# Kernel tuning notes

Measured on AMD Instinct MI355X. Metric: run time of the kernel, lower is better.

Reference implementation:

```python
import jax, jax.numpy as jnp
import numpy as np

B, N, D = 4, 2048, 1024
H = 16
HD = D // H


def setup_inputs() -> dict:
    key = jax.random.key(0)
    ks = jax.random.split(key, 7)
    bound_w = 1.0 / np.sqrt(D)  # kaiming_uniform(a=sqrt(5)) on (D, D) -> U(-1/sqrt(fan_in), 1/sqrt(fan_in))
    x = jax.random.normal(ks[0], (B, N, D), dtype=jnp.float32)
    Wq = jax.random.uniform(ks[1], (D, D), jnp.float32, -bound_w, bound_w)
    Wk = jax.random.uniform(ks[2], (D, D), jnp.float32, -bound_w, bound_w)
    Wv = jax.random.uniform(ks[3], (D, D), jnp.float32, -bound_w, bound_w)
    Wo = jax.random.uniform(ks[4], (D, D), jnp.float32, -bound_w, bound_w)
    bo = jax.random.uniform(ks[5], (D,), jnp.float32, -bound_w, bound_w)
    return {"x": x, "Wq": Wq, "Wk": Wk, "Wv": Wv, "Wo": Wo, "bo": bo}


def reference(x, Wq, Wk, Wv, Wo, bo):
    b, n, _ = x.shape
    # QKV projections: contraction over W's FIRST axis, matching torch einsum 'bnd,di->bni'
    Q = jnp.einsum('bnd,di->bni', x, Wq)
    K = jnp.einsum('bnd,di->bni', x, Wk)
    V = jnp.einsum('bnd,di->bni', x, Wv)
    # split heads: [b, h, n, hd]
    Q = Q.reshape(b, n, H, HD).transpose(0, 2, 1, 3)
    K = K.reshape(b, n, H, HD).transpose(0, 2, 1, 3)
    V = V.reshape(b, n, H, HD).transpose(0, 2, 1, 3)
    scores = jnp.einsum('bhnd,bhmd->bhnm', Q, K) / np.sqrt(HD).astype(np.float32)
    causal = jnp.triu(jnp.ones((n, n), dtype=bool), k=1)  # True above diagonal -> masked
    scores = jnp.where(causal[None, None, :, :], -jnp.inf, scores)
    attn = jax.nn.softmax(scores, axis=-1)
    # dropout rate is 0.0 -> identity
    ctx = jnp.einsum('bhnm,bhmd->bhnd', attn, V)
    ctx = ctx.transpose(0, 2, 1, 3).reshape(b, n, D)
    return ctx @ Wo.T + bo
```

## Files before the change

### kernel.cpp

```cpp
#include <hip/hip_runtime.h>
#include <hip/hip_bf16.h>

typedef __bf16 bf16;
typedef __bf16 bf16x4 __attribute__((ext_vector_type(4)));
typedef __bf16 bf16x8 __attribute__((ext_vector_type(8)));
typedef float  f32x4  __attribute__((ext_vector_type(4)));

#define B_  4
#define N_  2048
#define D_  1024
#define H_  16
#define HD_ 64

#define QSCALE 0.1803368801111204f

__device__ __forceinline__ bf16x8 ld8(const bf16* p) {
  return *reinterpret_cast<const bf16x8*>(p);
}

__device__ __forceinline__ void gload16(const bf16* g, bf16* l) {
  __builtin_amdgcn_global_load_lds(
      (const __attribute__((address_space(1))) void*)g,
      (__attribute__((address_space(3))) void*)l, 16, 0, 0);
}

__global__ __launch_bounds__(256) void cast_k(const float* __restrict__ in,
                                              bf16* __restrict__ out, int n) {
  int i = (blockIdx.x * 256 + threadIdx.x) * 8;
  if (i >= n) return;
  float4 a = *reinterpret_cast<const float4*>(in + i);
  float4 b = *reinterpret_cast<const float4*>(in + i + 4);
  bf16x8 o;
  o[0] = (bf16)a.x; o[1] = (bf16)a.y; o[2] = (bf16)a.z; o[3] = (bf16)a.w;
  o[4] = (bf16)b.x; o[5] = (bf16)b.y; o[6] = (bf16)b.z; o[7] = (bf16)b.w;
  *reinterpret_cast<bf16x8*>(out + i) = o;
}

__global__ __launch_bounds__(1024)
void transpose3_k(const float* __restrict__ w0, const float* __restrict__ w1,
                  const float* __restrict__ w2, bf16* __restrict__ out) {
  __shared__ float t[32][33];
  const int z = blockIdx.z;
  const float* in = (z == 0) ? w0 : (z == 1) ? w1 : w2;
  const float scale = (z == 0) ? QSCALE : 1.0f;
  bf16* o = out + (size_t)z * D_ * D_;
  int c = blockIdx.x * 32 + threadIdx.x;
  int r = blockIdx.y * 32 + threadIdx.y;
  t[threadIdx.y][threadIdx.x] = in[r * D_ + c];
  __syncthreads();
  int oc = blockIdx.y * 32 + threadIdx.x;
  int orr = blockIdx.x * 32 + threadIdx.y;
  o[orr * D_ + oc] = (bf16)(scale * t[threadIdx.x][threadIdx.y]);
}

#define GEMM_CORE(A_, Bt_, K_)                                                    \
  f32x4 acc[4][4] = {};                                                           \
  const int srow = wid * 16 + (lane >> 2);                \
  const int schk = ((lane & 3) ^ ((lane >> 4) & 3)) * 8;         \
  const int q8   = ((lane >> 4) ^ (l15 >> 2)) * 8;              \
  _Pragma("unroll")                                                               \
  for (int j = 0; j < 2; ++j) {                                                   \
    gload16(&(A_)[(size_t)(brow + j * 64 + srow) * (K_) + schk],                  \
            &As[(j * 64 + wid * 16) * 32]);                                       \
    gload16(&(Bt_)[(size_t)(bcol + j * 64 + srow) * (K_) + schk],                 \
            &Bs[(j * 64 + wid * 16) * 32]);                                       \
  }                                                                               \
  _Pragma("unroll")                                                               \
  for (int j = 0; j < 2; ++j) {                                                   \
    gload16(&(A_)[(size_t)(brow + j * 64 + srow) * (K_) + 32 + schk],             \
            &As[4096 + (j * 64 + wid * 16) * 32]);                                \
    gload16(&(Bt_)[(size_t)(bcol + j * 64 + srow) * (K_) + 32 + schk],            \
            &Bs[4096 + (j * 64 + wid * 16) * 32]);                                \
  }                                                                               \
  const int NIT = (K_) / 32;                                                      \
  int cur = 0, pre = 2;                                                           \
  for (int t = 0; t < NIT; ++t) {                                                 \
    asm volatile("s_barrier" ::: "memory");             \
    __builtin_amdgcn_sched_barrier(0);                                            \
    if (t + 2 < NIT) {                                                            \
      const int kk = (t + 2) * 32;                                                \
      _Pragma("unroll")                                                           \
      for (int j = 0; j < 2; ++j) {                                               \
        gload16(&(A_)[(size_t)(brow + j * 64 + srow) * (K_) + kk + schk],         \
                &As[pre * 4096 + (j * 64 + wid * 16) * 32]);                      \
        gload16(&(Bt_)[(size_t)(bcol + j * 64 + srow) * (K_) + kk + schk],        \
                &Bs[pre * 4096 + (j * 64 + wid * 16) * 32]);                      \
      }                                                                           \
      asm volatile("s_waitcnt vmcnt(8)" ::: "memory");                            \
    } else if (t + 1 < NIT) {                                                     \
      asm volatile("s_waitcnt vmcnt(4)" ::: "memory");                            \
    } else {                                                                      \
      asm volatile("s_waitcnt vmcnt(0)" ::: "memory");                            \
    }                                                                             \
    asm volatile("s_barrier" ::: "memory");             \
    __builtin_amdgcn_sched_barrier(0);                                            \
    const bf16* Ac = &As[cur * 4096];                                             \
    const bf16* Bc = &Bs[cur * 4096];                                             \
    bf16x8 af[4], bfr[4];                                                         \
    _Pragma("unroll")                                                             \
    for (int m = 0; m < 4; ++m)                                                   \
      af[m] = *reinterpret_cast<const bf16x8*>(&Ac[(wr + m * 16 + l15) * 32 + q8]); \
    _Pragma("unroll")                                                             \
    for (int n = 0; n < 4; ++n)                                                   \
      bfr[n] = *reinterpret_cast<const bf16x8*>(&Bc[(wc + n * 16 + l15) * 32 + q8]); \
    _Pragma("unroll")                                                             \
    for (int m = 0; m < 4; ++m)                                                   \
      _Pragma("unroll")                                                           \
      for (int n = 0; n < 4; ++n)                                                 \
        acc[m][n] = __builtin_amdgcn_mfma_f32_16x16x32_bf16(af[m], bfr[n],        \
                                                            acc[m][n], 0, 0, 0);  \
    cur = (cur == 2) ? 0 : cur + 1;                                               \
    pre = (pre == 2) ? 0 : pre + 1;                                               \
  }

__global__ __launch_bounds__(256, 3)
void gemm_qkv(const bf16* __restrict__ A, const bf16* __restrict__ Bt,
              bf16* __restrict__ qb, bf16* __restrict__ kb, bf16* __restrict__ vtb)
{
  __shared__ bf16 As[3 * 128 * 32];
  __shared__ bf16 Bs[3 * 128 * 32];
  const int tid  = threadIdx.x;
  const int lane = tid & 63;
  const int wid  = tid >> 6;
  const int wg   = blockIdx.x;
  const int xcd  = wg & 7;
  const int idx  = wg >> 3;
  const int brow = ((xcd << 3) + (idx & 7)) * 128;
  const int bcol = (idx >> 3) * 128;
  const int wr   = (wid >> 1) * 64;
  const int wc   = (wid & 1) * 64;
  const int l15  = lane & 15;
  const int g    = lane >> 4;

  GEMM_CORE(A, Bt, D_)

  const int which = bcol >> 10;
  const int r0 = g * 4;
  if (which == 2) {
#pragma unroll
    for (int m = 0; m < 4; ++m)
#pragma unroll
      for (int n = 0; n < 4; ++n) {
        int nn0  = brow + wr + m * 16 + r0;
        int gcol = (bcol & 1023) + wc + n * 16 + l15;
        int b = nn0 >> 11, nn = nn0 & (N_ - 1);
        int h = gcol >> 6, hd = gcol & 63;
        bf16x4 o;
#pragma unroll
        for (int r = 0; r < 4; ++r) o[r] = (bf16)acc[m][n][r];
        *reinterpret_cast<bf16x4*>(
            &vtb[((size_t)((b * H_ + h) * HD_ + hd)) * N_ + nn]) = o;
      }
  } else {
    bf16* outp = (which == 0) ? qb : kb;
#pragma unroll
    for (int m = 0; m < 4; ++m)
#pragma unroll
      for (int n = 0; n < 4; ++n)
#pragma unroll
        for (int r = 0; r < 4; ++r) {
          int grow = brow + wr + m * 16 + r0 + r;
          int gcol = (bcol & 1023) + wc + n * 16 + l15;
          int b = grow >> 11, nn = grow & (N_ - 1);
          int h = gcol >> 6, hd = gcol & 63;
          outp[((((size_t)(b * H_ + h)) * N_ + nn) << 6) + hd] = (bf16)acc[m][n][r];
        }
  }
}

__global__ __launch_bounds__(256, 3)
void gemm_out(const bf16* __restrict__ A, const bf16* __restrict__ Bt,
              float* __restrict__ C, const float* __restrict__ bias)
{
  __shared__ bf16 As[3 * 128 * 32];
  __shared__ bf16 Bs[3 * 128 * 32];
  const int tid  = threadIdx.x;
  const int lane = tid & 63;
  const int wid  = tid >> 6;
  const int wg   = blockIdx.x;
  const int xcd  = wg & 7;
  const int idx  = wg >> 3;
  const int brow = ((xcd << 3) + (idx & 7)) * 128;
  const int bcol = (idx >> 3) * 128;
  const int wr   = (wid >> 1) * 64;
  const int wc   = (wid & 1) * 64;
  const int l15  = lane & 15;
  const int g    = lane >> 4;

  GEMM_CORE(A, Bt, D_)

  const int r0 = g * 4;
#pragma unroll
  for (int m = 0; m < 4; ++m)
#pragma unroll
    for (int n = 0; n < 4; ++n)
#pragma unroll
      for (int r = 0; r < 4; ++r) {
        int grow = brow + wr + m * 16 + r0 + r;
        int gcol = bcol + wc + n * 16 + l15;
        C[(size_t)grow * D_ + gcol] = acc[m][n][r] + bias[gcol];
      }
}

__global__ __launch_bounds__(256, 3)
void attn_k(const bf16* __restrict__ q, const bf16* __restrict__ k,
            const bf16* __restrict__ vt, bf16* __restrict__ ctx)
{
  __shared__ bf16 Ks[2][64 * 64];
  __shared__ bf16 Vs[2][64 * 64];
  __shared__ bf16 Pl[4][2][16][72];
  const int tid  = threadIdx.x;
  const int lane = tid & 63;
  const int wid  = tid >> 6;
  const int bid  = blockIdx.x;
  const int bh   = bid & 63;
  const int c    = 15 - (bid >> 6);
  const int l15  = lane & 15;
  const int g    = lane >> 4;
  const int lk   = g * 8;
  const int swz  = (l15 & 7) << 4;

  const bf16* kp = k  + (size_t)bh * N_ * HD_;
  const bf16* vp = vt + (size_t)bh * HD_ * N_;
  const int b = bh >> 4, h = bh & 15;

  const int sr8   = lane >> 3;
  const int scoff = ((lane & 7) ^ sr8) * 8;

  bf16x8 ones8;
#pragma unroll
  for (int i = 0; i < 8; ++i) ones8[i] = (bf16)1.0f;

  const int qbase = c * 128 + wid * 32;
  const int nt    = 2 * c + 2;
  const int tm    = 2 * c + (wid >> 1);

  const bf16* qp = q + ((size_t)bh * N_ + qbase) * HD_;
  bf16x8 aq[2][2];
#pragma unroll
  for (int m = 0; m < 2; ++m)
#pragma unroll
    for (int c2 = 0; c2 < 2; ++c2)
      aq[m][c2] = ld8(qp + (size_t)(m * 16 + l15) * HD_ + c2 * 32 + lk);

  f32x4 oacc[2][5] = {};

#pragma unroll
  for (int j = 0; j < 2; ++j) {
    const int rr = j * 32 + wid * 8 + sr8;
    gload16(kp + (size_t)rr * HD_ + scoff, &Ks[0][(j * 32 + wid * 8) * 64]);
    gload16(vp + (size_t)rr * N_ + scoff, &Vs[0][(j * 32 + wid * 8) * 64]);
  }

  for (int t = 0; t < nt; ++t) {
    const int cur = t & 1;
    asm volatile("s_barrier" ::: "memory");
    __builtin_amdgcn_sched_barrier(0);
    if (t + 1 < nt) {
      const int kb = (t + 1) * 64;
#pragma unroll
      for (int j = 0; j < 2; ++j) {
        const int rr = j * 32 + wid * 8 + sr8;
        gload16(kp + (size_t)(kb + rr) * HD_ + scoff,
                &Ks[cur ^ 1][(j * 32 + wid * 8) * 64]);
        gload16(vp + (size_t)rr * N_ + kb + scoff,
                &Vs[cur ^ 1][(j * 32 + wid * 8) * 64]);
      }
      asm volatile("s_waitcnt vmcnt(4)" ::: "memory");
    } else {
      asm volatile("s_waitcnt vmcnt(0)" ::: "memory");
    }
    asm volatile("s_barrier" ::: "memory");
    __builtin_amdgcn_sched_barrier(0);

    if (t <= tm) {
      const char* kb_ = (const char*)&Ks[cur][0];
      const char* vb_ = (const char*)&Vs[cur][0];

      f32x4 s[2][4] = {};
#pragma unroll
      for (int tt = 0; tt < 4; ++tt) {
        bf16x8 bk0 = *reinterpret_cast<const bf16x8*>(
            kb_ + (tt * 16 + l15) * 128 + ((g * 16) ^ swz));
        bf16x8 bk1 = *reinterpret_cast<const bf16x8*>(
            kb_ + (tt * 16 + l15) * 128 + ((64 + g * 16) ^ swz));
#pragma unroll
        for (int m = 0; m < 2; ++m) {
          s[m][tt] = __builtin_amdgcn_mfma_f32_16x16x32_bf16(bk0, aq[m][0], s[m][tt], 0, 0, 0);
          s[m][tt] = __builtin_amdgcn_mfma_f32_16x16x32_bf16(bk1, aq[m][1], s[m][tt], 0, 0, 0);
        }
      }

      if (t == tm) {
#pragma unroll
        for (int m = 0; m < 2; ++m) {
          const int qr = qbase + m * 16 + l15;
#pragma unroll
          for (int tt = 0; tt < 4; ++tt)
#pragma unroll
            for (int r = 0; r < 4; ++r) {
              int kq = t * 64 + tt * 16 + g * 4 + r;
              if (kq > qr) s[m][tt][r] = -1e30f;
            }
        }
      }

#pragma unroll
      for (int m = 0; m < 2; ++m) {
#pragma unroll
        for (int tt = 0; tt < 4; ++tt)
#pragma unroll
          for (int r = 0; r < 4; ++r) s[m][tt][r] = exp2f(s[m][tt][r]);

#pragma unroll
        for (int tt = 0; tt < 4; ++tt) {
          bf16x4 pk;
#pragma unroll
          for (int r = 0; r < 4; ++r) pk[r] = (bf16)s[m][tt][r];
          *reinterpret_cast<bf16x4*>(&Pl[wid][m][l15][tt * 16 + g * 4]) = pk;
        }
      }

#pragma unroll
      for (int kc = 0; kc < 2; ++kc) {
        bf16x8 pb[2];
#pragma unroll
        for (int m = 0; m < 2; ++m)
          pb[m] = *reinterpret_cast<const bf16x8*>(&Pl[wid][m][l15][kc * 32 + lk]);
#pragma unroll
        for (int n = 0; n < 4; ++n) {
          bf16x8 vf = *reinterpret_cast<const bf16x8*>(
              vb_ + (n * 16 + l15) * 128 + ((kc * 64 + g * 16) ^ swz));
#pragma unroll
          for (int m = 0; m < 2; ++m)
            oacc[m][n] = __builtin_amdgcn_mfma_f32_16x16x32_bf16(vf, pb[m], oacc[m][n], 0, 0, 0);
        }
#pragma unroll
        for (int m = 0; m < 2; ++m)
          oacc[m][4] = __builtin_amdgcn_mfma_f32_16x16x32_bf16(ones8, pb[m], oacc[m][4], 0, 0, 0);
      }
    }
  }

#pragma unroll
  for (int m = 0; m < 2; ++m) {
    float inv = 1.f / oacc[m][4][0];
    bf16* cp = ctx + ((size_t)b * N_ + qbase + m * 16 + l15) * D_ + h * HD_;
#pragma unroll
    for (int n = 0; n < 4; ++n) {
      bf16x4 o;
#pragma unroll
      for (int r = 0; r < 4; ++r) o[r] = (bf16)(oacc[m][n][r] * inv);
      *reinterpret_cast<bf16x4*>(cp + n * 16 + g * 4) = o;
    }
  }
}

extern "C" void kernel_launch(void* const* d_in, const int* in_sizes, int n_in,
                              void* d_out, int out_size, void* d_ws, size_t ws_size,
                              hipStream_t stream)
{
  const float* x  = (const float*)d_in[0];
  const float* Wq = (const float*)d_in[1];
  const float* Wk = (const float*)d_in[2];
  const float* Wv = (const float*)d_in[3];
  const float* Wo = (const float*)d_in[4];
  const float* bo = (const float*)d_in[5];
  float* out = (float*)d_out;

  const size_t SZ_BHND = (size_t)B_ * H_ * N_ * HD_ * sizeof(bf16);
  const size_t SZ_W    = (size_t)D_ * D_ * sizeof(bf16);
  char* ws = (char*)d_ws;
  bf16* xbf  = (bf16*)(ws);
  bf16* ctx  = (bf16*)(ws);
  bf16* qb   = (bf16*)(ws + SZ_BHND);
  bf16* kbf  = (bf16*)(ws + 2 * SZ_BHND);
  bf16* vtb  = (bf16*)(ws + 3 * SZ_BHND);
  bf16* wqkv = (bf16*)(ws + 4 * SZ_BHND);
  bf16* wob  = (bf16*)(ws + 4 * SZ_BHND + 3 * SZ_W);
  if (ws_size < 4 * SZ_BHND + 4 * SZ_W) return;

  const int NX = B_ * N_ * D_;
  cast_k<<<NX / (256 * 8), 256, 0, stream>>>(x, xbf, NX);
  cast_k<<<(D_ * D_) / (256 * 8), 256, 0, stream>>>(Wo, wob, D_ * D_);

  transpose3_k<<<dim3(32, 32, 3), dim3(32, 32), 0, stream>>>(Wq, Wk, Wv, wqkv);

  gemm_qkv<<<1536, 256, 0, stream>>>(xbf, wqkv, qb, kbf, vtb);

  attn_k<<<1024, 256, 0, stream>>>(qb, kbf, vtb, ctx);

  gemm_out<<<512, 256, 0, stream>>>(ctx, wob, out, bo);
}
```

Baseline: 169.1 us.

## Enlarge QKV GEMM tile to 256x128 with 8 waves and raw exp2 in attention

The QKV projection GEMM now uses 512-thread blocks computing 256x128 output tiles, with double buffering instead of triple buffering and a remapped block-to-tile index. Each B tile is loaded once and shared by twice as many rows, which is meant to cut global and LDS traffic per FLOP and halve the block count. The shared GEMM macro is inlined into gemm_out unchanged. Separately, the attention softmax calls v_exp_f32 directly in place of exp2f, dropping the library's range and denormal handling. The shallower prefetch depth and larger blocks may expose more memory latency, and the raw exp skips special-case handling.

```diff
diff --git a/kernel.cpp b/kernel.cpp
--- a/kernel.cpp
+++ b/kernel.cpp
@@ -16,6 +16,12 @@
 
 __device__ __forceinline__ bf16x8 ld8(const bf16* p) {
   return *reinterpret_cast<const bf16x8*>(p);
+}
+
+__device__ __forceinline__ float exp2_raw(float x) {
+  float y;
+  asm("v_exp_f32 %0, %1" : "=v"(y) : "v"(x));
+  return y;
 }
 
 __device__ __forceinline__ void gload16(const bf16* g, bf16* l) {
@@ -53,86 +59,72 @@
   o[orr * D_ + oc] = (bf16)(scale * t[threadIdx.x][threadIdx.y]);
 }
 
-#define GEMM_CORE(A_, Bt_, K_)                                                    \
-  f32x4 acc[4][4] = {};                                                           \
-  const int srow = wid * 16 + (lane >> 2);                \
-  const int schk = ((lane & 3) ^ ((lane >> 4) & 3)) * 8;         \
-  const int q8   = ((lane >> 4) ^ (l15 >> 2)) * 8;              \
-  _Pragma("unroll")                                                               \
-  for (int j = 0; j < 2; ++j) {                                                   \
-    gload16(&(A_)[(size_t)(brow + j * 64 + srow) * (K_) + schk],                  \
-            &As[(j * 64 + wid * 16) * 32]);                                       \
-    gload16(&(Bt_)[(size_t)(bcol + j * 64 + srow) * (K_) + schk],                 \
-            &Bs[(j * 64 + wid * 16) * 32]);                                       \
-  }                                                                               \
-  _Pragma("unroll")                                                               \
-  for (int j = 0; j < 2; ++j) {                                                   \
-    gload16(&(A_)[(size_t)(brow + j * 64 + srow) * (K_) + 32 + schk],             \
-            &As[4096 + (j * 64 + wid * 16) * 32]);                                \
-    gload16(&(Bt_)[(size_t)(bcol + j * 64 + srow) * (K_) + 32 + schk],            \
-            &Bs[4096 + (j * 64 + wid * 16) * 32]);                                \
-  }                                                                               \
-  const int NIT = (K_) / 32;                                                      \
-  int cur = 0, pre = 2;                                                           \
-  for (int t = 0; t < NIT; ++t) {                                                 \
-    asm volatile("s_barrier" ::: "memory");             \
-    __builtin_amdgcn_sched_barrier(0);                                            \
-    if (t + 2 < NIT) {                                                            \
-      const int kk = (t + 2) * 32;                                                \
-      _Pragma("unroll")                                                           \
-      for (int j = 0; j < 2; ++j) {                                               \
-        gload16(&(A_)[(size_t)(brow + j * 64 + srow) * (K_) + kk + schk],         \
-                &As[pre * 4096 + (j * 64 + wid * 16) * 32]);                      \
-        gload16(&(Bt_)[(size_t)(bcol + j * 64 + srow) * (K_) + kk + schk],        \
-                &Bs[pre * 4096 + (j * 64 + wid * 16) * 32]);                      \
-      }                                                                           \
-      asm volatile("s_waitcnt vmcnt(8)" ::: "memory");                            \
-    } else if (t + 1 < NIT) {                                                     \
-      asm volatile("s_waitcnt vmcnt(4)" ::: "memory");                            \
-    } else {                                                                      \
-      asm volatile("s_waitcnt vmcnt(0)" ::: "memory");                            \
-    }                                                                             \
-    asm volatile("s_barrier" ::: "memory");             \
-    __builtin_amdgcn_sched_barrier(0);                                            \
-    const bf16* Ac = &As[cur * 4096];                                             \
-    const bf16* Bc = &Bs[cur * 4096];                                             \
-    bf16x8 af[4], bfr[4];                                                         \
-    _Pragma("unroll")                                                             \
-    for (int m = 0; m < 4; ++m)                                                   \
-      af[m] = *reinterpret_cast<const bf16x8*>(&Ac[(wr + m * 16 + l15) * 32 + q8]); \
-    _Pragma("unroll")                                                             \
-    for (int n = 0; n < 4; ++n)                                                   \
-      bfr[n] = *reinterpret_cast<const bf16x8*>(&Bc[(wc + n * 16 + l15) * 32 + q8]); \
-    _Pragma("unroll")                                                             \
-    for (int m = 0; m < 4; ++m)                                                   \
-      _Pragma("unroll")                                                           \
-      for (int n = 0; n < 4; ++n)                                                 \
-        acc[m][n] = __builtin_amdgcn_mfma_f32_16x16x32_bf16(af[m], bfr[n],        \
-                                                            acc[m][n], 0, 0, 0);  \
-    cur = (cur == 2) ? 0 : cur + 1;                                               \
-    pre = (pre == 2) ? 0 : pre + 1;                                               \
-  }
-
-__global__ __launch_bounds__(256, 3)
+__global__ __launch_bounds__(512, 6)
 void gemm_qkv(const bf16* __restrict__ A, const bf16* __restrict__ Bt,
               bf16* __restrict__ qb, bf16* __restrict__ kb, bf16* __restrict__ vtb)
 {
-  __shared__ bf16 As[3 * 128 * 32];
-  __shared__ bf16 Bs[3 * 128 * 32];
+  __shared__ bf16 As[2 * 256 * 32];
+  __shared__ bf16 Bs[2 * 128 * 32];
   const int tid  = threadIdx.x;
   const int lane = tid & 63;
   const int wid  = tid >> 6;
   const int wg   = blockIdx.x;
   const int xcd  = wg & 7;
   const int idx  = wg >> 3;
-  const int brow = ((xcd << 3) + (idx & 7)) * 128;
-  const int bcol = (idx >> 3) * 128;
+  const int brow = ((xcd << 2) + (idx & 3)) * 256;
+  const int bcol = (idx >> 2) * 128;
   const int wr   = (wid >> 1) * 64;
   const int wc   = (wid & 1) * 64;
   const int l15  = lane & 15;
   const int g    = lane >> 4;
 
-  GEMM_CORE(A, Bt, D_)
+  f32x4 acc[4][4] = {};
+  const int srow = wid * 16 + (lane >> 2);
+  const int schk = ((lane & 3) ^ ((lane >> 4) & 3)) * 8;
+  const int q8   = ((lane >> 4) ^ (l15 >> 2)) * 8;
+
+#pragma unroll
+  for (int j = 0; j < 2; ++j)
+    gload16(&A[(size_t)(brow + j * 128 + srow) * D_ + schk],
+            &As[(j * 128 + wid * 16) * 32]);
+  gload16(&Bt[(size_t)(bcol + srow) * D_ + schk], &Bs[(wid * 16) * 32]);
+
+  const int NIT = D_ / 32;
+  for (int t = 0; t < NIT; ++t) {
+    const int cur = t & 1;
+    asm volatile("s_barrier" ::: "memory");
+    __builtin_amdgcn_sched_barrier(0);
+    if (t + 1 < NIT) {
+      const int kk = (t + 1) * 32;
+#pragma unroll
+      for (int j = 0; j < 2; ++j)
+        gload16(&A[(size_t)(brow + j * 128 + srow) * D_ + kk + schk],
+                &As[(cur ^ 1) * 8192 + (j * 128 + wid * 16) * 32]);
+      gload16(&Bt[(size_t)(bcol + srow) * D_ + kk + schk],
+              &Bs[(cur ^ 1) * 4096 + (wid * 16) * 32]);
+      asm volatile("s_waitcnt vmcnt(3)" ::: "memory");
+    } else {
+      asm volatile("s_waitcnt vmcnt(0)" ::: "memory");
+    }
+    asm volatile("s_barrier" ::: "memory");
+    __builtin_amdgcn_sched_barrier(0);
+
+    const bf16* Ac = &As[cur * 8192];
+    const bf16* Bc = &Bs[cur * 4096];
+    bf16x8 af[4], bfr[4];
+#pragma unroll
+    for (int m = 0; m < 4; ++m)
+      af[m] = *reinterpret_cast<const bf16x8*>(&Ac[(wr + m * 16 + l15) * 32 + q8]);
+#pragma unroll
+    for (int n = 0; n < 4; ++n)
+      bfr[n] = *reinterpret_cast<const bf16x8*>(&Bc[(wc + n * 16 + l15) * 32 + q8]);
+#pragma unroll
+    for (int m = 0; m < 4; ++m)
+#pragma unroll
+      for (int n = 0; n < 4; ++n)
+        acc[m][n] = __builtin_amdgcn_mfma_f32_16x16x32_bf16(af[m], bfr[n],
+                                                            acc[m][n], 0, 0, 0);
+  }
 
   const int which = bcol >> 10;
   const int r0 = g * 4;
@@ -187,7 +179,64 @@
   const int l15  = lane & 15;
   const int g    = lane >> 4;
 
-  GEMM_CORE(A, Bt, D_)
+  f32x4 acc[4][4] = {};
+  const int srow = wid * 16 + (lane >> 2);
+  const int schk = ((lane & 3) ^ ((lane >> 4) & 3)) * 8;
+  const int q8   = ((lane >> 4) ^ (l15 >> 2)) * 8;
+#pragma unroll
+  for (int j = 0; j < 2; ++j) {
+    gload16(&A[(size_t)(brow + j * 64 + srow) * D_ + schk],
+            &As[(j * 64 + wid * 16) * 32]);
+    gload16(&Bt[(size_t)(bcol + j * 64 + srow) * D_ + schk],
+            &Bs[(j * 64 + wid * 16) * 32]);
+  }
+#pragma unroll
+  for (int j = 0; j < 2; ++j) {
+    gload16(&A[(size_t)(brow + j * 64 + srow) * D_ + 32 + schk],
+            &As[4096 + (j * 64 + wid * 16) * 32]);
+    gload16(&Bt[(size_t)(bcol + j * 64 + srow) * D_ + 32 + schk],
+            &Bs[4096 + (j * 64 + wid * 16) * 32]);
+  }
+  const int NIT = D_ / 32;
+  int cur = 0, pre = 2;
+  for (int t = 0; t < NIT; ++t) {
+    asm volatile("s_barrier" ::: "memory");
+    __builtin_amdgcn_sched_barrier(0);
+    if (t + 2 < NIT) {
+      const int kk = (t + 2) * 32;
+#pragma unroll
+      for (int j = 0; j < 2; ++j) {
+        gload16(&A[(size_t)(brow + j * 64 + srow) * D_ + kk + schk],
+                &As[pre * 4096 + (j * 64 + wid * 16) * 32]);
+        gload16(&Bt[(size_t)(bcol + j * 64 + srow) * D_ + kk + schk],
+                &Bs[pre * 4096 + (j * 64 + wid * 16) * 32]);
+      }
+      asm volatile("s_waitcnt vmcnt(8)" ::: "memory");
+    } else if (t + 1 < NIT) {
+      asm volatile("s_waitcnt vmcnt(4)" ::: "memory");
+    } else {
+      asm volatile("s_waitcnt vmcnt(0)" ::: "memory");
+    }
+    asm volatile("s_barrier" ::: "memory");
+    __builtin_amdgcn_sched_barrier(0);
+    const bf16* Ac = &As[cur * 4096];
+    const bf16* Bc = &Bs[cur * 4096];
+    bf16x8 af[4], bfr[4];
+#pragma unroll
+    for (int m = 0; m < 4; ++m)
+      af[m] = *reinterpret_cast<const bf16x8*>(&Ac[(wr + m * 16 + l15) * 32 + q8]);
+#pragma unroll
+    for (int n = 0; n < 4; ++n)
+      bfr[n] = *reinterpret_cast<const bf16x8*>(&Bc[(wc + n * 16 + l15) * 32 + q8]);
+#pragma unroll
+    for (int m = 0; m < 4; ++m)
+#pragma unroll
+      for (int n = 0; n < 4; ++n)
+        acc[m][n] = __builtin_amdgcn_mfma_f32_16x16x32_bf16(af[m], bfr[n],
+                                                            acc[m][n], 0, 0, 0);
+    cur = (cur == 2) ? 0 : cur + 1;
+    pre = (pre == 2) ? 0 : pre + 1;
+  }
 
   const int r0 = g * 4;
 #pragma unroll
@@ -310,7 +359,7 @@
 #pragma unroll
         for (int tt = 0; tt < 4; ++tt)
 #pragma unroll
-          for (int r = 0; r < 4; ++r) s[m][tt][r] = exp2f(s[m][tt][r]);
+          for (int r = 0; r < 4; ++r) s[m][tt][r] = exp2_raw(s[m][tt][r]);
 
 #pragma unroll
         for (int tt = 0; tt < 4; ++tt) {
@@ -386,7 +435,7 @@
 
   transpose3_k<<<dim3(32, 32, 3), dim3(32, 32), 0, stream>>>(Wq, Wk, Wv, wqkv);
 
-  gemm_qkv<<<1536, 256, 0, stream>>>(xbf, wqkv, qb, kbf, vtb);
+  gemm_qkv<<<768, 512, 0, stream>>>(xbf, wqkv, qb, kbf, vtb);
 
   attn_k<<<1024, 256, 0, stream>>>(qb, kbf, vtb, ctx);
 
```

Result: slower. 352.3 us (+108.3%).
